# Kernel tuning notes

Measured on AMD Instinct MI355X. Metric: run time of the kernel, lower is better.

The kernel has to match this reference:

```python
import jax, jax.numpy as jnp
import numpy as np

B, C, H, W, WS, SH, NH, P = 64, 512, 28, 28, 7, 3, 16, 10
MLP_H = 2048
EPS = 1e-5
NW = (H // WS) * (W // WS)  # 16 windows per image
N = P + WS * WS             # 59 tokens per window
HEAD_D = C // NH
SCALE = HEAD_D ** -0.5


def _rel_pos_index(ws):
    coords = np.stack(np.meshgrid(np.arange(ws), np.arange(ws), indexing='ij')).reshape(2, -1)
    rel = (coords[:, :, None] - coords[:, None, :]).transpose(1, 2, 0)
    rel[..., 0] += ws - 1
    rel[..., 1] += ws - 1
    rel[..., 0] *= 2 * ws - 1
    return rel.sum(-1)  # (ws*ws, ws*ws)


def _attn_mask(h, w, ws, shift):
    img = np.zeros((h, w), dtype=np.float32)
    slices = (slice(0, -ws), slice(-ws, -shift), slice(-shift, None))
    cnt = 0
    for hs in slices:
        for wsl in slices:
            img[hs, wsl] = cnt
            cnt += 1
    mw = img.reshape(h // ws, ws, w // ws, ws).transpose(0, 2, 1, 3).reshape(-1, ws * ws)
    diff = mw[:, None, :] - mw[:, :, None]
    return np.where(diff != 0, -100.0, 0.0).astype(np.float32)  # (nW, ws*ws, ws*ws)


_RPI = jnp.asarray(_rel_pos_index(WS))
_MASK = jnp.asarray(_attn_mask(H, W, WS, SH))


def _ln(x, g, b):
    mu = jnp.mean(x, -1, keepdims=True)
    var = jnp.mean((x - mu) ** 2, -1, keepdims=True)
    return (x - mu) * jax.lax.rsqrt(var + EPS) * g + b


def _window_partition(x, ws):
    b, h, w, c = x.shape
    x = x.reshape(b, h // ws, ws, w // ws, ws, c).transpose(0, 1, 3, 2, 4, 5)
    return x.reshape(-1, ws, ws, c)


def _window_reverse(win, ws, h, w):
    b = win.shape[0] // ((h // ws) * (w // ws))
    x = win.reshape(b, h // ws, w // ws, ws, ws, -1).transpose(0, 1, 3, 2, 4, 5)
    return x.reshape(b, h, w, -1)


def setup_inputs() -> dict:
    key = jax.random.key(0)
    ks = jax.random.split(key, 8)
    d = {
        'x': jax.random.normal(ks[0], (B, P + H * W, C), jnp.float32),
        'g1': jnp.ones((C,), jnp.float32),
        'b1': jnp.zeros((C,), jnp.float32),
        'qkv_w': jax.random.normal(ks[1], (3 * C, C), jnp.float32) * 0.02,
        'qkv_b': jnp.zeros((3 * C,), jnp.float32),
        'rpb_table': jax.random.normal(ks[2], ((2 * WS - 1) ** 2, NH), jnp.float32) * 0.02,
        'proj_w': jax.random.normal(ks[3], (C, C), jnp.float32) * 0.02,
        'proj_b': jnp.zeros((C,), jnp.float32),
        'g2': jnp.ones((C,), jnp.float32),
        'b2': jnp.zeros((C,), jnp.float32),
        'fc1_w': jax.random.normal(ks[4], (MLP_H, C), jnp.float32) * 0.02,
        'fc1_b': jnp.zeros((MLP_H,), jnp.float32),
        'fc2_w': jax.random.normal(ks[5], (C, MLP_H), jnp.float32) * 0.02,
        'fc2_b': jnp.zeros((C,), jnp.float32),
    }
    return d


def _block(x, g1, b1, qkv_w, qkv_b, rpb_table, proj_w, proj_b, g2, b2, fc1_w, fc1_b, fc2_w, fc2_b):
    prompt = x[:, :P, :]                       # (B, P, C)
    x = x[:, P:, :]                            # (B, H*W, C)
    shortcut = x
    xn = _ln(x, g1, b1).reshape(B, H, W, C)
    # cyclic shift
    xn = jnp.roll(xn, shift=(-SH, -SH), axis=(1, 2))
    xw = _window_partition(xn, WS).reshape(-1, WS * WS, C)  # (B*nW, 49, C)
    # prompt padding (matches torch expand(nW,...).reshape order: index = w*B + b)
    pw = jnp.broadcast_to(prompt[None], (NW, B, P, C)).reshape(-1, P, C)
    xw = jnp.concatenate([pw, xw], axis=1)     # (B*nW, N, C)
    B_ = B * NW
    # attention
    qkv = (xw @ qkv_w.T + qkv_b).reshape(B_, N, 3, NH, HEAD_D).transpose(2, 0, 3, 1, 4)
    q, k, v = qkv[0], qkv[1], qkv[2]
    attn = jnp.einsum('bhnd,bhmd->bhnm', q * SCALE, k)  # (B_, NH, N, N)
    bias = rpb_table[_RPI.reshape(-1)].reshape(WS * WS, WS * WS, NH).transpose(2, 0, 1)
    bias = jnp.pad(bias, ((0, 0), (P, 0), (P, 0)))       # (NH, N, N)
    mask = jnp.pad(_MASK, ((0, 0), (P, 0), (P, 0)))      # (nW, N, N)
    attn = attn + bias[None]
    attn = attn.reshape(B, NW, NH, N, N) + mask[None, :, None]
    attn = jax.nn.softmax(attn.reshape(B_, NH, N, N), axis=-1)
    out = jnp.einsum('bhnm,bhmd->bhnd', attn, v).transpose(0, 2, 1, 3).reshape(B_, N, C)
    out = out @ proj_w.T + proj_b
    # drop prompts, un-window, un-shift
    out = out[:, P:, :].reshape(-1, WS, WS, C)
    xs = _window_reverse(out, WS, H, W)
    xs = jnp.roll(xs, shift=(SH, SH), axis=(1, 2)).reshape(B, H * W, C)
    x = shortcut + xs
    # MLP (exact GELU, as torch nn.GELU)
    h = _ln(x, g2, b2)
    h = jax.nn.gelu(h @ fc1_w.T + fc1_b, approximate=False)
    h = h @ fc2_w.T + fc2_b
    return x + h


def reference(x, g1, b1, qkv_w, qkv_b, rpb_table, proj_w, proj_b, g2, b2, fc1_w, fc1_b, fc2_w, fc2_b):
    return _block(x, g1, b1, qkv_w, qkv_b, rpb_table, proj_w, proj_b, g2, b2, fc1_w, fc1_b, fc2_w, fc2_b)
```

## Files before the change

### kernel.cpp

```cpp
#include <hip/hip_runtime.h>
#include <stdint.h>

typedef unsigned short u16;
typedef unsigned int u32;
typedef __attribute__((ext_vector_type(8))) short short8;
typedef __attribute__((ext_vector_type(4))) float f32x4;

__device__ __forceinline__ u16 f2bf(float f) {
  u32 u = __builtin_bit_cast(u32, f);
  u32 r = u + 0x7FFFu + ((u >> 16) & 1u);
  return (u16)(r >> 16);
}

__device__ __forceinline__ void gl_lds16(const void* g, void* l) {
  __builtin_amdgcn_global_load_lds((__attribute__((address_space(1))) void*)g,
                                   (__attribute__((address_space(3))) void*)l,
                                   16, 0, 0);
}

__global__ __launch_bounds__(256) void cvt_bf16(const float* __restrict__ in,
                                                u16* __restrict__ out, int n4) {
  int idx = blockIdx.x * 256 + threadIdx.x;
  if (idx < n4) {
    float4 v = ((const float4*)in)[idx];
    u32 lo = (u32)f2bf(v.x) | ((u32)f2bf(v.y) << 16);
    u32 hi = (u32)f2bf(v.z) | ((u32)f2bf(v.w) << 16);
    ((uint2*)out)[idx] = make_uint2(lo, hi);
  }
}

__global__ __launch_bounds__(256) void ln1_kernel(const float* __restrict__ x,
                                                  const float* __restrict__ g,
                                                  const float* __restrict__ bta,
                                                  u16* __restrict__ xcat) {
  int wave = threadIdx.x >> 6, lane = threadIdx.x & 63;
  int row = blockIdx.x * 4 + wave;
  const float* src;
  bool do_ln;
  if (row < 640) {
    int bb = row / 10, p = row - bb * 10;
    src = x + ((size_t)bb * 794 + p) * 512;
    do_ln = false;
  } else {
    int r2 = row - 640;
    int i = r2 / 49, t = r2 - i * 49;
    int bb = i >> 4, nw = i & 15;
    int tr = t / 7, tc = t - tr * 7;
    int hh = (nw >> 2) * 7 + tr + 3; if (hh >= 28) hh -= 28;
    int ww = (nw & 3) * 7 + tc + 3;  if (ww >= 28) ww -= 28;
    src = x + ((size_t)bb * 794 + 10 + hh * 28 + ww) * 512;
    do_ln = true;
  }
  float4 v0 = ((const float4*)src)[lane * 2];
  float4 v1 = ((const float4*)src)[lane * 2 + 1];
  float vals[8] = {v0.x, v0.y, v0.z, v0.w, v1.x, v1.y, v1.z, v1.w};
  u16 ob[8];
  if (do_ln) {
    float s = 0.f, s2 = 0.f;
#pragma unroll
    for (int j = 0; j < 8; ++j) { s += vals[j]; s2 += vals[j] * vals[j]; }
#pragma unroll
    for (int o = 32; o > 0; o >>= 1) { s += __shfl_xor(s, o); s2 += __shfl_xor(s2, o); }
    float mu = s * (1.0f / 512.0f);
    float var = s2 * (1.0f / 512.0f) - mu * mu;
    float inv = rsqrtf(var + 1e-5f);
    float4 ga = ((const float4*)g)[lane * 2], gb = ((const float4*)g)[lane * 2 + 1];
    float4 ba = ((const float4*)bta)[lane * 2], bb2 = ((const float4*)bta)[lane * 2 + 1];
    float gv[8] = {ga.x, ga.y, ga.z, ga.w, gb.x, gb.y, gb.z, gb.w};
    float bv[8] = {ba.x, ba.y, ba.z, ba.w, bb2.x, bb2.y, bb2.z, bb2.w};
#pragma unroll
    for (int j = 0; j < 8; ++j) ob[j] = f2bf((vals[j] - mu) * inv * gv[j] + bv[j]);
  } else {
#pragma unroll
    for (int j = 0; j < 8; ++j) ob[j] = f2bf(vals[j]);
  }
  u32 w0 = (u32)ob[0] | ((u32)ob[1] << 16);
  u32 w1 = (u32)ob[2] | ((u32)ob[3] << 16);
  u32 w2 = (u32)ob[4] | ((u32)ob[5] << 16);
  u32 w3 = (u32)ob[6] | ((u32)ob[7] << 16);
  ((uint4*)(xcat + (size_t)row * 512))[lane] = make_uint4(w0, w1, w2, w3);
}

__global__ __launch_bounds__(256) void ln2_kernel(const float* __restrict__ xn,
                                                  const float* __restrict__ g,
                                                  const float* __restrict__ bta,
                                                  u16* __restrict__ outb) {
  int wave = threadIdx.x >> 6, lane = threadIdx.x & 63;
  size_t row = (size_t)blockIdx.x * 4 + wave;
  const float* src = xn + row * 512;
  float4 v0 = ((const float4*)src)[lane * 2];
  float4 v1 = ((const float4*)src)[lane * 2 + 1];
  float vals[8] = {v0.x, v0.y, v0.z, v0.w, v1.x, v1.y, v1.z, v1.w};
  float s = 0.f, s2 = 0.f;
#pragma unroll
  for (int j = 0; j < 8; ++j) { s += vals[j]; s2 += vals[j] * vals[j]; }
#pragma unroll
  for (int o = 32; o > 0; o >>= 1) { s += __shfl_xor(s, o); s2 += __shfl_xor(s2, o); }
  float mu = s * (1.0f / 512.0f);
  float var = s2 * (1.0f / 512.0f) - mu * mu;
  float inv = rsqrtf(var + 1e-5f);
  float4 ga = ((const float4*)g)[lane * 2], gb = ((const float4*)g)[lane * 2 + 1];
  float4 ba = ((const float4*)bta)[lane * 2], bb2 = ((const float4*)bta)[lane * 2 + 1];
  float gv[8] = {ga.x, ga.y, ga.z, ga.w, gb.x, gb.y, gb.z, gb.w};
  float bv[8] = {ba.x, ba.y, ba.z, ba.w, bb2.x, bb2.y, bb2.z, bb2.w};
  u16 ob[8];
#pragma unroll
  for (int j = 0; j < 8; ++j) ob[j] = f2bf((vals[j] - mu) * inv * gv[j] + bv[j]);
  u32 w0 = (u32)ob[0] | ((u32)ob[1] << 16);
  u32 w1 = (u32)ob[2] | ((u32)ob[3] << 16);
  u32 w2 = (u32)ob[4] | ((u32)ob[5] << 16);
  u32 w3 = (u32)ob[6] | ((u32)ob[7] << 16);
  ((uint4*)(outb + row * 512))[lane] = make_uint4(w0, w1, w2, w3);
}

template <int EPI>
__global__ __launch_bounds__(256) void gemm128(const u16* __restrict__ A,
                                               const u16* __restrict__ Wt,
                                               const float* __restrict__ bias,
                                               u16* __restrict__ outb,
                                               float* __restrict__ outf,
                                               const float* __restrict__ res,
                                               int M, int N, int K) {
  __shared__ __align__(16) u16 Al[128 * 32];
  __shared__ __align__(16) u16 Bl[128 * 32];
  const int tid = threadIdx.x;
  const int lane = tid & 63;
  const int wv = tid >> 6;
  const int wm = wv >> 1, wn = wv & 1;
  const int tm = blockIdx.y * 128, tn = blockIdx.x * 128;
  const int lr = lane & 15;
  const int lk = (lane >> 4) * 8;

  f32x4 acc[4][4];
#pragma unroll
  for (int m = 0; m < 4; ++m)
#pragma unroll
    for (int n = 0; n < 4; ++n)
#pragma unroll
      for (int r2 = 0; r2 < 4; ++r2) acc[m][n][r2] = 0.f;

  const int rA = tid >> 2;
  const int kA = (tid & 3) * 8;
  const u16* Abase = A + (size_t)(tm + rA) * K + kA;
  const u16* Bbase = Wt + (size_t)(tn + rA) * K + kA;
  const size_t k64 = (size_t)64 * K;

  for (int k0 = 0; k0 < K; k0 += 32) {
    gl_lds16(Abase + k0, &Al[tid * 8]);
    gl_lds16(Abase + k64 + k0, &Al[2048 + tid * 8]);
    gl_lds16(Bbase + k0, &Bl[tid * 8]);
    gl_lds16(Bbase + k64 + k0, &Bl[2048 + tid * 8]);
    __syncthreads();
    short8 af[4], bf[4];
#pragma unroll
    for (int m = 0; m < 4; ++m)
      af[m] = *(const short8*)&Al[(wm * 64 + m * 16 + lr) * 32 + lk];
#pragma unroll
    for (int n = 0; n < 4; ++n)
      bf[n] = *(const short8*)&Bl[(wn * 64 + n * 16 + lr) * 32 + lk];
#pragma unroll
    for (int m = 0; m < 4; ++m)
#pragma unroll
      for (int n = 0; n < 4; ++n)
        acc[m][n] = __builtin_amdgcn_mfma_f32_16x16x32_bf16(af[m], bf[n], acc[m][n], 0, 0, 0);
    __syncthreads();
  }

  float bcol[4];
#pragma unroll
  for (int n = 0; n < 4; ++n) bcol[n] = bias[tn + wn * 64 + n * 16 + lr];

#pragma unroll
  for (int m = 0; m < 4; ++m) {
#pragma unroll
    for (int r2 = 0; r2 < 4; ++r2) {
      int grow = tm + wm * 64 + m * 16 + (lane >> 4) * 4 + r2;
      if (EPI == 1) {
        int i = grow / 49, t = grow - i * 49;
        int bb = i >> 4, nw = i & 15;
        int tr = t / 7, tc = t - tr * 7;
        int hh = (nw >> 2) * 7 + tr + 3; if (hh >= 28) hh -= 28;
        int ww = (nw & 3) * 7 + tc + 3;  if (ww >= 28) ww -= 28;
        size_t dstr = ((size_t)bb * 784 + hh * 28 + ww) * 512;
        size_t srcr = ((size_t)bb * 794 + 10 + hh * 28 + ww) * 512;
#pragma unroll
        for (int n = 0; n < 4; ++n) {
          int gcol = tn + wn * 64 + n * 16 + lr;
          float v = acc[m][n][r2] + bcol[n];
          outf[dstr + gcol] = v + res[srcr + gcol];
        }
      } else {
#pragma unroll
        for (int n = 0; n < 4; ++n) {
          int gcol = tn + wn * 64 + n * 16 + lr;
          float v = acc[m][n][r2] + bcol[n];
          if (EPI == 0) {
            outb[(size_t)grow * N + gcol] = f2bf(v);
          } else if (EPI == 2) {
            float gel = 0.5f * v * (1.0f + erff(v * 0.70710678118654752f));
            outb[(size_t)grow * N + gcol] = f2bf(gel);
          } else {
            outf[(size_t)grow * N + gcol] = v + res[(size_t)grow * 512 + gcol];
          }
        }
      }
    }
  }
}

__global__ __launch_bounds__(64) void attn_kernel(const u16* __restrict__ Y,
                                                  const float* __restrict__ rpb,
                                                  u16* __restrict__ outp) {
  __shared__ __align__(16) u16 Plds[64 * 64];
  __shared__ __align__(16) u16 Vt[32 * 64];
  __shared__ float biasl[169];
  const int lane = threadIdx.x;
  const int i = blockIdx.x >> 4;
  const int hd = blockIdx.x & 15;
  const int bp = i & 63;
  const int nw = i & 15;
  const int hi = nw >> 2, wi = nw & 3;
  const int lr = lane & 15;
  const int lk = (lane >> 4) * 8;

  for (int j = lane; j < 169; j += 64) biasl[j] = rpb[j * 16 + hd];

  short8 qf[4], kf[4];
#pragma unroll
  for (int m = 0; m < 4; ++m) {
    int t = m * 16 + lr;
    size_t r = (t < 10) ? (size_t)(bp * 10 + t) : (size_t)(640 + i * 49 + (t - 10));
    const u16* base = Y + r * 1536 + hd * 32 + lk;
    if (t < 59) {
      qf[m] = *(const short8*)(base);
      kf[m] = *(const short8*)(base + 512);
    } else {
#pragma unroll
      for (int e = 0; e < 8; ++e) { qf[m][e] = 0; kf[m][e] = 0; }
    }
  }
  {
    int t = lane;
    if (t < 59) {
      size_t r = (t < 10) ? (size_t)(bp * 10 + t) : (size_t)(640 + i * 49 + (t - 10));
      const u16* vp = Y + r * 1536 + 1024 + hd * 32;
      short8 vv0 = *(const short8*)(vp);
      short8 vv1 = *(const short8*)(vp + 8);
      short8 vv2 = *(const short8*)(vp + 16);
      short8 vv3 = *(const short8*)(vp + 24);
#pragma unroll
      for (int e = 0; e < 8; ++e) {
        Vt[e * 64 + t] = (u16)vv0[e];
        Vt[(8 + e) * 64 + t] = (u16)vv1[e];
        Vt[(16 + e) * 64 + t] = (u16)vv2[e];
        Vt[(24 + e) * 64 + t] = (u16)vv3[e];
      }
    } else {
      for (int d = 0; d < 32; ++d) Vt[d * 64 + t] = 0;
    }
  }

  f32x4 s[4][4];
#pragma unroll
  for (int m = 0; m < 4; ++m)
#pragma unroll
    for (int n = 0; n < 4; ++n)
#pragma unroll
      for (int r2 = 0; r2 < 4; ++r2) s[m][n][r2] = 0.f;
#pragma unroll
  for (int m = 0; m < 4; ++m)
#pragma unroll
    for (int n = 0; n < 4; ++n)
      s[m][n] = __builtin_amdgcn_mfma_f32_16x16x32_bf16(qf[m], kf[n], s[m][n], 0, 0, 0);

  __syncthreads();

  const float SCALE = 0.17677669529663687f;
  const int rgrp = lane >> 4;
#pragma unroll
  for (int m = 0; m < 4; ++m) {
#pragma unroll
    for (int r2 = 0; r2 < 4; ++r2) {
      int rn = m * 16 + rgrp * 4 + r2;
      int qa = rn - 10;
      int qra = qa / 7, qca = qa - qra * 7;
      int regA = 0;
      if (qa >= 0 && qa < 49) {
        int ha = hi * 7 + qra, wa = wi * 7 + qca;
        regA = (ha < 21 ? 0 : (ha < 25 ? 1 : 2)) * 3 + (wa < 21 ? 0 : (wa < 25 ? 1 : 2));
      }
      float vloc[4];
      float mx = -3.0e38f;
#pragma unroll
      for (int n = 0; n < 4; ++n) {
        int cm = n * 16 + lr;
        float v;
        if (cm >= 59) {
          v = -3.0e38f;
        } else {
          v = s[m][n][r2] * SCALE;
          if (rn >= 10 && rn < 59 && cm >= 10) {
            int kb = cm - 10;
            int krb = kb / 7, kcb = kb - krb * 7;
            v += biasl[(qra - krb + 6) * 13 + (qca - kcb + 6)];
            int hb = hi * 7 + krb, wb = wi * 7 + kcb;
            int regB = (hb < 21 ? 0 : (hb < 25 ? 1 : 2)) * 3 + (wb < 21 ? 0 : (wb < 25 ? 1 : 2));
            if (regA != regB) v -= 100.0f;
          }
        }
        vloc[n] = v;
        mx = fmaxf(mx, v);
      }
#pragma unroll
      for (int o = 8; o > 0; o >>= 1) mx = fmaxf(mx, __shfl_xor(mx, o));
      float sum = 0.f;
#pragma unroll
      for (int n = 0; n < 4; ++n) {
        float e = __expf(vloc[n] - mx);
        vloc[n] = e;
        sum += e;
      }
#pragma unroll
      for (int o = 8; o > 0; o >>= 1) sum += __shfl_xor(sum, o);
      float inv = 1.0f / sum;
#pragma unroll
      for (int n = 0; n < 4; ++n)
        Plds[rn * 64 + n * 16 + lr] = f2bf(vloc[n] * inv);
    }
  }

  __syncthreads();

  f32x4 o[4][2];
#pragma unroll
  for (int m = 0; m < 4; ++m)
#pragma unroll
    for (int j = 0; j < 2; ++j)
#pragma unroll
      for (int r2 = 0; r2 < 4; ++r2) o[m][j][r2] = 0.f;
#pragma unroll
  for (int ks = 0; ks < 2; ++ks) {
    short8 pf[4], vf[2];
#pragma unroll
    for (int m = 0; m < 4; ++m)
      pf[m] = *(const short8*)&Plds[(m * 16 + lr) * 64 + ks * 32 + lk];
#pragma unroll
    for (int j = 0; j < 2; ++j)
      vf[j] = *(const short8*)&Vt[(j * 16 + lr) * 64 + ks * 32 + lk];
#pragma unroll
    for (int m = 0; m < 4; ++m)
#pragma unroll
      for (int j = 0; j < 2; ++j)
        o[m][j] = __builtin_amdgcn_mfma_f32_16x16x32_bf16(pf[m], vf[j], o[m][j], 0, 0, 0);
  }

#pragma unroll
  for (int m = 0; m < 4; ++m) {
#pragma unroll
    for (int r2 = 0; r2 < 4; ++r2) {
      int rn = m * 16 + rgrp * 4 + r2;
      if (rn >= 10 && rn < 59) {
        size_t row = (size_t)i * 49 + (rn - 10);
        u16* op = outp + row * 512 + hd * 32;
        op[lr] = f2bf(o[m][0][r2]);
        op[16 + lr] = f2bf(o[m][1][r2]);
      }
    }
  }
}

extern "C" void kernel_launch(void* const* d_in, const int* in_sizes, int n_in,
                              void* d_out, int out_size, void* d_ws, size_t ws_size,
                              hipStream_t stream) {
  const float* x = (const float*)d_in[0];
  const float* g1 = (const float*)d_in[1];
  const float* b1 = (const float*)d_in[2];
  const float* qkv_w = (const float*)d_in[3];
  const float* qkv_b = (const float*)d_in[4];
  const float* rpb = (const float*)d_in[5];
  const float* proj_w = (const float*)d_in[6];
  const float* proj_b = (const float*)d_in[7];
  const float* g2 = (const float*)d_in[8];
  const float* b2 = (const float*)d_in[9];
  const float* fc1_w = (const float*)d_in[10];
  const float* fc1_b = (const float*)d_in[11];
  const float* fc2_w = (const float*)d_in[12];
  const float* fc2_b = (const float*)d_in[13];
  float* out = (float*)d_out;

  char* ws = (char*)d_ws;
  u16* qkv_wb = (u16*)(ws + 0);
  u16* proj_wb = (u16*)(ws + 1572864);
  u16* fc1_wb = (u16*)(ws + 2097152);
  u16* fc2_wb = (u16*)(ws + 4194304);
  u16* xcat = (u16*)(ws + 6291456);
  u16* y = (u16*)(ws + 58327040);
  u16* attnv = (u16*)(ws + 214433792);
  float* xnew = (float*)(ws + 265814016);
  u16* hin = xcat;
  u16* hmid = y;

  cvt_bf16<<<768, 256, 0, stream>>>(qkv_w, qkv_wb, 196608);
  cvt_bf16<<<256, 256, 0, stream>>>(proj_w, proj_wb, 65536);
  cvt_bf16<<<1024, 256, 0, stream>>>(fc1_w, fc1_wb, 262144);
  cvt_bf16<<<1024, 256, 0, stream>>>(fc2_w, fc2_wb, 262144);

  ln1_kernel<<<12704, 256, 0, stream>>>(x, g1, b1, xcat);

  gemm128<0><<<dim3(12, 397), 256, 0, stream>>>(xcat, qkv_wb, qkv_b, y, nullptr, nullptr,
                                                50816, 1536, 512);

  attn_kernel<<<16384, 64, 0, stream>>>(y, rpb, attnv);

  gemm128<1><<<dim3(4, 392), 256, 0, stream>>>(attnv, proj_wb, proj_b, nullptr, xnew, x,
                                               50176, 512, 512);

  ln2_kernel<<<12544, 256, 0, stream>>>(xnew, g2, b2, hin);

  gemm128<2><<<dim3(16, 392), 256, 0, stream>>>(hin, fc1_wb, fc1_b, hmid, nullptr, nullptr,
                                                50176, 2048, 512);

  gemm128<3><<<dim3(4, 392), 256, 0, stream>>>(hmid, fc2_wb, fc2_b, nullptr, out, xnew,
                                               50176, 512, 2048);
}
```

Measured before the change: 812.3 us.

## Triple-buffer LDS in gemm128 to overlap global loads with MFMA

Replaces the single-buffered K loop of the bf16 GEMM with a three-stage LDS ring. Two tiles are prefetched ahead using global_load_lds, and an explicit vmcnt wait plus one barrier per iteration replaces the two __syncthreads per step. The goal is to hide global-memory latency behind the MFMA work and cut barrier overhead. In exchange, LDS use per block triples to 48KB, which may reduce occupancy.

```diff
diff --git a/kernel.cpp b/kernel.cpp
--- a/kernel.cpp
+++ b/kernel.cpp
@@ -121,8 +121,8 @@
                                                float* __restrict__ outf,
                                                const float* __restrict__ res,
                                                int M, int N, int K) {
-  __shared__ __align__(16) u16 Al[128 * 32];
-  __shared__ __align__(16) u16 Bl[128 * 32];
+  __shared__ __align__(16) u16 Al[3][128 * 32];
+  __shared__ __align__(16) u16 Bl[3][128 * 32];
   const int tid = threadIdx.x;
   const int lane = tid & 63;
   const int wv = tid >> 6;
@@ -144,27 +144,48 @@
   const u16* Abase = A + (size_t)(tm + rA) * K + kA;
   const u16* Bbase = Wt + (size_t)(tn + rA) * K + kA;
   const size_t k64 = (size_t)64 * K;
-
-  for (int k0 = 0; k0 < K; k0 += 32) {
-    gl_lds16(Abase + k0, &Al[tid * 8]);
-    gl_lds16(Abase + k64 + k0, &Al[2048 + tid * 8]);
-    gl_lds16(Bbase + k0, &Bl[tid * 8]);
-    gl_lds16(Bbase + k64 + k0, &Bl[2048 + tid * 8]);
-    __syncthreads();
+  const int NT = K >> 5;
+
+#define STAGE(buf, kk)                                          \
+  do {                                                          \
+    gl_lds16(Abase + (kk), &Al[buf][tid * 8]);                  \
+    gl_lds16(Abase + k64 + (kk), &Al[buf][2048 + tid * 8]);     \
+    gl_lds16(Bbase + (kk), &Bl[buf][tid * 8]);                  \
+    gl_lds16(Bbase + k64 + (kk), &Bl[buf][2048 + tid * 8]);     \
+  } while (0)
+
+  STAGE(0, 0);
+  STAGE(1, 32);
+
+  int cur = 0;
+  for (int t = 0; t < NT; ++t) {
+    if (t < NT - 1) asm volatile("s_waitcnt vmcnt(4)" ::: "memory");
+    else            asm volatile("s_waitcnt vmcnt(0)" ::: "memory");
+    __builtin_amdgcn_s_barrier();
+    asm volatile("" ::: "memory");
+
+    if (t + 2 < NT) {
+      int nb = cur + 2; if (nb >= 3) nb -= 3;
+      STAGE(nb, (t + 2) * 32);
+    }
+
     short8 af[4], bf[4];
 #pragma unroll
     for (int m = 0; m < 4; ++m)
-      af[m] = *(const short8*)&Al[(wm * 64 + m * 16 + lr) * 32 + lk];
+      af[m] = *(const short8*)&Al[cur][(wm * 64 + m * 16 + lr) * 32 + lk];
 #pragma unroll
     for (int n = 0; n < 4; ++n)
-      bf[n] = *(const short8*)&Bl[(wn * 64 + n * 16 + lr) * 32 + lk];
+      bf[n] = *(const short8*)&Bl[cur][(wn * 64 + n * 16 + lr) * 32 + lk];
 #pragma unroll
     for (int m = 0; m < 4; ++m)
 #pragma unroll
       for (int n = 0; n < 4; ++n)
         acc[m][n] = __builtin_amdgcn_mfma_f32_16x16x32_bf16(af[m], bf[n], acc[m][n], 0, 0, 0);
-    __syncthreads();
-  }
+
+    asm volatile("" ::: "memory");
+    cur = cur + 1; if (cur >= 3) cur -= 3;
+  }
+#undef STAGE
 
   float bcol[4];
 #pragma unroll
```

Measured after the change: 763.5 us. 1.06x faster.
